# Kernel tuning notes

Measured on AMD Instinct MI355X. Metric: run time of the kernel, lower is better.

Reference implementation:

```python
import jax, jax.numpy as jnp
import numpy as np

B = 64          # batch_size
H = 16384       # n_hidden
BS = 32         # block size of BlockSparseLinear
NB = H // BS    # 512 blocks per dim
NNZ = int(0.1 * NB * NB)  # 26214 nonzero blocks (density 0.1)
N_IN = 1024     # n_inputs
N_OUT = 1024    # n_outputs
STEPS = 8       # n_forward_steps


def setup_inputs() -> dict:
    key = jax.random.key(0)
    k1, k2, k3, k4, k5 = jax.random.split(key, 5)
    # kaiming-ish scale for effective fan-in = H * density
    w_scale = 1.0 / np.sqrt(H * 0.1)
    inp = jax.random.normal(k1, (B, N_IN), dtype=jnp.float32)
    blocks = jax.random.normal(k2, (NNZ, BS, BS), dtype=jnp.float32) * w_scale
    bias = jax.random.normal(k3, (H,), dtype=jnp.float32) * 0.01
    block_rows = jax.random.randint(k4, (NNZ,), 0, NB, dtype=jnp.int32)
    block_cols = jax.random.randint(k5, (NNZ,), 0, NB, dtype=jnp.int32)
    return {"inp": inp, "blocks": blocks, "bias": bias,
            "block_rows": block_rows, "block_cols": block_cols}


def _block_sparse_linear(blocks, block_rows, block_cols, bias, x):
    # x: [B, H] -> y = W_sparse @ x + bias, W stored as NNZ 32x32 blocks
    xb = x.reshape(B, NB, BS)[:, block_cols]               # [B, NNZ, BS]
    contrib = jnp.einsum('nij,bnj->nbi', blocks, xb)       # [NNZ, B, BS]
    yb = jax.ops.segment_sum(contrib, block_rows, num_segments=NB)  # [NB, B, BS]
    return yb.transpose(1, 0, 2).reshape(B, H) + bias


def reference(inp, blocks, bias, block_rows, block_cols):
    # hs = zeros[B, H]; first n_inputs slots get the input (squeeze trailing 1-dim)
    hs = jnp.zeros((B, H), dtype=inp.dtype).at[:, :N_IN].set(inp)
    for step in range(STEPS):
        hs = _block_sparse_linear(blocks, block_rows, block_cols, bias, hs)
        if step != STEPS - 1:
            hs = jax.nn.sigmoid(hs)
    # output_act = sigmoid on last n_outputs entries
    return jax.nn.sigmoid(hs[:, -N_OUT:])
```

## Files before the change

kernel.cpp:

```cpp
#include <hip/hip_runtime.h>
#include <stdint.h>

#define B_     64
#define H_     16384
#define NB_    512
#define NNZ_   26214
#define N_IN_  1024
#define N_OUT_ 1024

typedef __attribute__((ext_vector_type(8))) short    bf16x8;
typedef __attribute__((ext_vector_type(4))) float    f32x4;
typedef __attribute__((ext_vector_type(4))) unsigned int u32x4;

__device__ __forceinline__ unsigned short f2bf(float f) {
    union { unsigned int i; float f; } v; v.f = f;
    unsigned int x = v.i;
    return (unsigned short)((x + 0x7fffu + ((x >> 16) & 1u)) >> 16);
}

__device__ __forceinline__ bf16x8 ldfrag(const unsigned short* p) {
    union { u32x4 u; bf16x8 b; } cv;
    cv.u = *(const u32x4*)p;
    return cv.b;
}


__global__ void zero_cnt(int* __restrict__ cnt) { cnt[threadIdx.x] = 0; }

__global__ void hist(const int* __restrict__ rows, int* __restrict__ cnt) {
    int n = blockIdx.x * 256 + threadIdx.x;
    if (n < NNZ_) atomicAdd(&cnt[rows[n]], 1);
}

__global__ void scan_k(int* __restrict__ cnt, int* __restrict__ ptr) {
    __shared__ int tmp[NB_];
    int t = threadIdx.x;
    tmp[t] = cnt[t];
    __syncthreads();
    for (int off = 1; off < NB_; off <<= 1) {
        int v = (t >= off) ? tmp[t - off] : 0;
        __syncthreads();
        tmp[t] += v;
        __syncthreads();
    }
    if (t == 0) ptr[0] = 0;
    ptr[t + 1] = tmp[t];
    cnt[t] = 0;
}

__global__ void scatter2(const int* __restrict__ rows, const int* __restrict__ cols,
                         const int* __restrict__ ptr, int* __restrict__ cnt,
                         int2* __restrict__ pair2) {
    int n = blockIdx.x * 256 + threadIdx.x;
    if (n < NNZ_) {
        int r = rows[n];
        int pos = ptr[r] + atomicAdd(&cnt[r], 1);
        pair2[pos] = make_int2(n, cols[n]);
    }
}


__global__ __launch_bounds__(256) void conv_w(const float* __restrict__ w,
                                              unsigned short* __restrict__ wb,
                                              const int2* __restrict__ pair2) {
    int pos = blockIdx.x;
    int t   = threadIdx.x;
    int n   = pair2[pos].x;
    f32x4 v = __builtin_nontemporal_load((const f32x4*)(w + (size_t)n * 1024) + t);
    union { unsigned short s[4]; uint2 d; } o;
    o.s[0] = f2bf(v[0]); o.s[1] = f2bf(v[1]); o.s[2] = f2bf(v[2]); o.s[3] = f2bf(v[3]);
    ((uint2*)(wb + (size_t)pos * 1024))[t] = o.d;
}


__global__ __launch_bounds__(256) void init_x(const float* __restrict__ inp,
                                              unsigned short* __restrict__ xb) {
    int idx = blockIdx.x * 256 + threadIdx.x;
    int c = idx >> 11;
    int b = (idx >> 5) & 63;
    int j = idx & 31;
    int h = c * 32 + j;
    xb[idx] = (h < N_IN_) ? f2bf(inp[b * N_IN_ + h]) : (unsigned short)0;
}


#define MFMA8(A, Bv)                                                         \
    do {                                                                     \
        _Pragma("unroll")                                                    \
        for (int mt = 0; mt < 2; ++mt)                                       \
            _Pragma("unroll")                                                \
            for (int nt = 0; nt < 4; ++nt)                                   \
                acc[mt][nt] = __builtin_amdgcn_mfma_f32_16x16x32_bf16(       \
                                  A[mt], Bv[nt], acc[mt][nt], 0, 0, 0);      \
    } while (0)

#define REDUCE_EPILOGUE(LASTF)                                               \
    do {                                                                     \
        if (wv >= 4) {                                                       \
            _Pragma("unroll")                                                \
            for (int mt = 0; mt < 2; ++mt)                                   \
                _Pragma("unroll")                                            \
                for (int nt = 0; nt < 4; ++nt)                               \
                    _Pragma("unroll")                                        \
                    for (int q2 = 0; q2 < 4; ++q2)                           \
                        s_red[wv - 4][nt * 16 + half][mt * 16 + quad * 4 + q2] = \
                            acc[mt][nt][q2];                                 \
        }                                                                    \
        __syncthreads();                                                     \
        if (wv < 4) {                                                        \
            _Pragma("unroll")                                                \
            for (int mt = 0; mt < 2; ++mt)                                   \
                _Pragma("unroll")                                            \
                for (int nt = 0; nt < 4; ++nt)                               \
                    _Pragma("unroll")                                        \
                    for (int q2 = 0; q2 < 4; ++q2)                           \
                        s_red[wv][nt * 16 + half][mt * 16 + quad * 4 + q2] += \
                            acc[mt][nt][q2];                                 \
        }                                                                    \
        __syncthreads();                                                     \
        const int b  = tid >> 3;                                             \
        const int i0 = (tid & 7) * 4;                                        \
        const float4 bv = *(const float4*)&bias[r * 32 + i0];                \
        float v[4] = {bv.x, bv.y, bv.z, bv.w};                               \
        _Pragma("unroll")                                                    \
        for (int w = 0; w < 4; ++w)                                          \
            _Pragma("unroll")                                                \
            for (int k = 0; k < 4; ++k)                                      \
                v[k] += s_red[w][b][i0 + k];                                 \
        if (LASTF) {                                                         \
            float4 o;                                                        \
            o.x = 1.0f / (1.0f + __expf(-v[0]));                             \
            o.y = 1.0f / (1.0f + __expf(-v[1]));                             \
            o.z = 1.0f / (1.0f + __expf(-v[2]));                             \
            o.w = 1.0f / (1.0f + __expf(-v[3]));                             \
            *(float4*)&out[(size_t)b * N_OUT_ +                              \
                           (r - (NB_ - N_OUT_ / 32)) * 32 + i0] = o;         \
        } else {                                                             \
            union { unsigned short s[4]; uint2 u; } o;                       \
            _Pragma("unroll")                                                \
            for (int k = 0; k < 4; ++k)                                      \
                o.s[k] = f2bf(1.0f / (1.0f + __expf(-v[k])));                \
            *(uint2*)&xout[((size_t)r * 64 + b) * 32 + i0] = o.u;            \
        }                                                                    \
    } while (0)


template <bool LAST>
__global__ __launch_bounds__(512, 4) void rowfull_k(
        const unsigned short* __restrict__ x,
        unsigned short* __restrict__ xout,
        float* __restrict__ out,
        const unsigned short* __restrict__ wb,
        const float* __restrict__ bias,
        const int2* __restrict__ pair2,
        const int* __restrict__ ptr,
        int row_base) {
    __shared__ float s_red[4][64][33];

    const int r    = blockIdx.x + row_base;
    const int tid  = threadIdx.x;
    const int wv   = tid >> 6;
    const int lane = tid & 63;
    const int half = lane & 15;
    const int quad = lane >> 4;

    const int beg = ptr[r], cnt = ptr[r + 1] - beg;
    const int c0 = __builtin_amdgcn_readfirstlane(beg + (cnt * wv) / 8);
    const int mv = __builtin_amdgcn_readfirstlane(beg + (cnt * (wv + 1)) / 8 - c0);

    int xoff = 0;
    if (lane < mv) xoff = pair2[c0 + lane].y * 2048;

    const int off16 = half * 32 + quad * 8;
    const unsigned short* wbase = wb + (size_t)c0 * 1024 + off16;

    f32x4 acc[2][4] = {};
    bf16x8 A0[2], B0[4], A1[2], B1[4], A2[2], B2[4];

    #define LDST(A, Bv, t)                                                   \
        do {                                                                 \
            int tt = ((t) < mv - 1) ? (t) : (mv - 1);                        \
            const unsigned short* wp = wbase + (size_t)tt * 1024;            \
            A[0] = ldfrag(wp);                                               \
            A[1] = ldfrag(wp + 512);                                         \
            int xo = __builtin_amdgcn_readlane(xoff, tt);                    \
            const unsigned short* xp = x + xo + off16;                       \
            Bv[0] = ldfrag(xp);                                              \
            Bv[1] = ldfrag(xp + 512);                                        \
            Bv[2] = ldfrag(xp + 1024);                                       \
            Bv[3] = ldfrag(xp + 1536);                                       \
        } while (0)

    if (mv > 0) {
        LDST(A0, B0, 0);
        LDST(A1, B1, 1);
        LDST(A2, B2, 2);
        int j = 0;
        while (j + 3 < mv) {
            MFMA8(A0, B0); LDST(A0, B0, j + 3);
            MFMA8(A1, B1); LDST(A1, B1, j + 4);
            MFMA8(A2, B2); LDST(A2, B2, j + 5);
            j += 3;
        }
        MFMA8(A0, B0);
        if (mv - j > 1) MFMA8(A1, B1);
        if (mv - j > 2) MFMA8(A2, B2);
    }
    #undef LDST

    REDUCE_EPILOGUE(LAST);
}


__global__ __launch_bounds__(512, 4) void rowstep0_k(
        const unsigned short* __restrict__ x,
        unsigned short* __restrict__ xout,
        const unsigned short* __restrict__ wb,
        const float* __restrict__ bias,
        const int2* __restrict__ pair2,
        const int* __restrict__ ptr) {
    __shared__ int2  s_pairs[8][64];
    __shared__ float s_red[4][64][33];
    float* __restrict__ out = nullptr;

    const int r    = blockIdx.x;
    const int tid  = threadIdx.x;
    const int wv   = tid >> 6;
    const int lane = tid & 63;
    const int half = lane & 15;
    const int quad = lane >> 4;

    const int beg = ptr[r], cnt = ptr[r + 1] - beg;
    const int c0 = beg + (cnt * wv) / 8;
    const int m  = beg + (cnt * (wv + 1)) / 8 - c0;

    int2 pc = make_int2(0, 0);
    bool valid = (lane < m);
    if (valid) {
        int c = pair2[c0 + lane].y;
        pc = make_int2(c0 + lane, c);
        valid = (c < N_IN_ / 32);
    }
    unsigned long long mask = __ballot(valid);
    if (valid) {
        int pos = __popcll(mask & ((1ull << lane) - 1ull));
        s_pairs[wv][pos] = pc;
    }
    const int mv = __popcll(mask);

    const int off16 = half * 32 + quad * 8;

    f32x4 acc[2][4] = {};
    bf16x8 A0[2], B0[4], A1[2], B1[4];

    #define LDFRAGS0(A, Bv, p)                                               \
        do {                                                                 \
            const unsigned short* wp = wb + (size_t)(p).x * 1024 + off16;    \
            A[0] = ldfrag(wp);                                               \
            A[1] = ldfrag(wp + 512);                                         \
            const unsigned short* xp = x + (size_t)(p).y * 2048 + off16;     \
            Bv[0] = ldfrag(xp);                                              \
            Bv[1] = ldfrag(xp + 512);                                        \
            Bv[2] = ldfrag(xp + 1024);                                       \
            Bv[3] = ldfrag(xp + 1536);                                       \
        } while (0)

    if (mv > 0) { int2 p = s_pairs[wv][0]; LDFRAGS0(A0, B0, p); }
    int j = 0;
    while (j + 2 <= mv) {
        { int2 p = s_pairs[wv][j + 1]; LDFRAGS0(A1, B1, p); }
        MFMA8(A0, B0);
        if (j + 2 < mv) { int2 p = s_pairs[wv][j + 2]; LDFRAGS0(A0, B0, p); }
        MFMA8(A1, B1);
        j += 2;
    }
    if (j < mv) MFMA8(A0, B0);
    #undef LDFRAGS0

    REDUCE_EPILOGUE(false);
}


extern "C" void kernel_launch(void* const* d_in, const int* in_sizes, int n_in,
                              void* d_out, int out_size, void* d_ws, size_t ws_size,
                              hipStream_t stream) {
    const float* inp    = (const float*)d_in[0];
    const float* blocks = (const float*)d_in[1];
    const float* bias   = (const float*)d_in[2];
    const int*   rows   = (const int*)d_in[3];
    const int*   cols   = (const int*)d_in[4];
    float*       out    = (float*)d_out;

    char* ws = (char*)d_ws;
    unsigned short* wbf = (unsigned short*)ws;
    unsigned short* x0  = (unsigned short*)(ws + 53686272u);
    unsigned short* x1  = (unsigned short*)(ws + 53686272u + 2097152u);
    char*  idxbase      = ws + 53686272u + 2u * 2097152u;
    int*   rowptr = (int*)(idxbase);
    int*   rowcnt = (int*)(idxbase + 4096);
    int2*  pair2  = (int2*)(idxbase + 8192);

    zero_cnt<<<1, NB_, 0, stream>>>(rowcnt);
    hist<<<(NNZ_ + 255) / 256, 256, 0, stream>>>(rows, rowcnt);
    scan_k<<<1, NB_, 0, stream>>>(rowcnt, rowptr);
    scatter2<<<(NNZ_ + 255) / 256, 256, 0, stream>>>(rows, cols, rowptr, rowcnt, pair2);

    conv_w<<<NNZ_, 256, 0, stream>>>(blocks, wbf, pair2);

    init_x<<<(B_ * H_) / 256, 256, 0, stream>>>(inp, x0);

    unsigned short* cur = x0;
    unsigned short* nxt = x1;
    rowstep0_k<<<NB_, 512, 0, stream>>>(cur, nxt, wbf, bias, pair2, rowptr);
    { unsigned short* t = cur; cur = nxt; nxt = t; }
    for (int s = 1; s < 7; ++s) {
        rowfull_k<false><<<NB_, 512, 0, stream>>>(cur, nxt, nullptr, wbf, bias,
                                                  pair2, rowptr, 0);
        unsigned short* t = cur; cur = nxt; nxt = t;
    }
    rowfull_k<true><<<N_OUT_ / 32, 512, 0, stream>>>(cur, nullptr, out, wbf, bias,
                                                     pair2, rowptr,
                                                     NB_ - N_OUT_ / 32);
}
```

Baseline: 311.4 us.

## Fuse all eight recurrent steps into one cooperative kernel with grid barriers

Replaces the per-step kernel launches with a single cooperative persistent kernel (one block per block-row) that loops over the eight steps and uses a hand-written atomic grid barrier between them. The four indexing kernels are merged into one single-block kernel using shared-memory atomics, and weight conversion and input init are merged into one launch. The steady-state pipeline depth also drops from three to two stages. This removes launch gaps and tail effects but relies on all 512 blocks being co-resident, and barrier spin costs may offset the savings.

Measured after the change: 765.2 us. 146% more time.

```diff
diff --git a/kernel.cpp b/kernel.cpp
--- a/kernel.cpp
+++ b/kernel.cpp
@@ -1,4 +1,5 @@
 #include <hip/hip_runtime.h>
+#include <hip/hip_cooperative_groups.h>
 #include <stdint.h>
 
 #define B_     64
@@ -25,62 +26,88 @@
 }
 
 
-__global__ void zero_cnt(int* __restrict__ cnt) { cnt[threadIdx.x] = 0; }
-
-__global__ void hist(const int* __restrict__ rows, int* __restrict__ cnt) {
-    int n = blockIdx.x * 256 + threadIdx.x;
-    if (n < NNZ_) atomicAdd(&cnt[rows[n]], 1);
-}
-
-__global__ void scan_k(int* __restrict__ cnt, int* __restrict__ ptr) {
-    __shared__ int tmp[NB_];
-    int t = threadIdx.x;
-    tmp[t] = cnt[t];
+__global__ __launch_bounds__(1024) void index_k(
+        const int* __restrict__ rows, const int* __restrict__ cols,
+        int* __restrict__ rowptr, int2* __restrict__ pair2,
+        int* __restrict__ bar) {
+    __shared__ int s_cnt[NB_];
+    __shared__ int s_off[NB_];
+    const int t = threadIdx.x;
+
+    if (t < NB_) s_cnt[t] = 0;
+    if (t < 64) bar[t] = 0;
     __syncthreads();
+
+    for (int n = t; n < NNZ_; n += 1024)
+        atomicAdd(&s_cnt[rows[n]], 1);
+    __syncthreads();
+
     for (int off = 1; off < NB_; off <<= 1) {
-        int v = (t >= off) ? tmp[t - off] : 0;
+        int v = 0;
+        if (t < NB_ && t >= off) v = s_cnt[t - off];
         __syncthreads();
-        tmp[t] += v;
+        if (t < NB_) s_cnt[t] += v;
         __syncthreads();
     }
-    if (t == 0) ptr[0] = 0;
-    ptr[t + 1] = tmp[t];
-    cnt[t] = 0;
-}
-
-__global__ void scatter2(const int* __restrict__ rows, const int* __restrict__ cols,
-                         const int* __restrict__ ptr, int* __restrict__ cnt,
-                         int2* __restrict__ pair2) {
-    int n = blockIdx.x * 256 + threadIdx.x;
-    if (n < NNZ_) {
+
+    if (t == 0) rowptr[0] = 0;
+    if (t < NB_) {
+        rowptr[t + 1] = s_cnt[t];
+        s_off[t] = (t == 0) ? 0 : s_cnt[t - 1];
+    }
+    __syncthreads();
+
+    for (int n = t; n < NNZ_; n += 1024) {
         int r = rows[n];
-        int pos = ptr[r] + atomicAdd(&cnt[r], 1);
+        int pos = atomicAdd(&s_off[r], 1);
         pair2[pos] = make_int2(n, cols[n]);
     }
 }
 
 
-__global__ __launch_bounds__(256) void conv_w(const float* __restrict__ w,
-                                              unsigned short* __restrict__ wb,
-                                              const int2* __restrict__ pair2) {
-    int pos = blockIdx.x;
-    int t   = threadIdx.x;
-    int n   = pair2[pos].x;
-    f32x4 v = __builtin_nontemporal_load((const f32x4*)(w + (size_t)n * 1024) + t);
-    union { unsigned short s[4]; uint2 d; } o;
-    o.s[0] = f2bf(v[0]); o.s[1] = f2bf(v[1]); o.s[2] = f2bf(v[2]); o.s[3] = f2bf(v[3]);
-    ((uint2*)(wb + (size_t)pos * 1024))[t] = o.d;
-}
-
-
-__global__ __launch_bounds__(256) void init_x(const float* __restrict__ inp,
-                                              unsigned short* __restrict__ xb) {
-    int idx = blockIdx.x * 256 + threadIdx.x;
-    int c = idx >> 11;
-    int b = (idx >> 5) & 63;
-    int j = idx & 31;
-    int h = c * 32 + j;
-    xb[idx] = (h < N_IN_) ? f2bf(inp[b * N_IN_ + h]) : (unsigned short)0;
+__global__ __launch_bounds__(256) void prep_k(
+        const float* __restrict__ w, unsigned short* __restrict__ wb,
+        const int2* __restrict__ pair2,
+        const float* __restrict__ inp, unsigned short* __restrict__ xb) {
+    const int bb = blockIdx.x;
+    if (bb < NNZ_) {
+        int t = threadIdx.x;
+        int n = pair2[bb].x;
+        f32x4 v = __builtin_nontemporal_load((const f32x4*)(w + (size_t)n * 1024) + t);
+        union { unsigned short s[4]; uint2 d; } o;
+        o.s[0] = f2bf(v[0]); o.s[1] = f2bf(v[1]);
+        o.s[2] = f2bf(v[2]); o.s[3] = f2bf(v[3]);
+        ((uint2*)(wb + (size_t)bb * 1024))[t] = o.d;
+    } else {
+        int idx = (bb - NNZ_) * 256 + threadIdx.x;
+        int c = idx >> 11;
+        int b = (idx >> 5) & 63;
+        int j = idx & 31;
+        int h = c * 32 + j;
+        xb[idx] = (h < N_IN_) ? f2bf(inp[b * N_IN_ + h]) : (unsigned short)0;
+    }
+}
+
+
+__device__ __forceinline__ void gbar(int* bar, int it) {
+    __syncthreads();
+    if (threadIdx.x == 0) {
+        __threadfence();
+        int a = __hip_atomic_fetch_add(&bar[0], 1, __ATOMIC_ACQ_REL,
+                                       __HIP_MEMORY_SCOPE_AGENT);
+        if (a == NB_ - 1) {
+            __hip_atomic_store(&bar[0], 0, __ATOMIC_RELAXED,
+                               __HIP_MEMORY_SCOPE_AGENT);
+            __hip_atomic_store(&bar[32], it + 1, __ATOMIC_RELEASE,
+                               __HIP_MEMORY_SCOPE_AGENT);
+        } else {
+            while (__hip_atomic_load(&bar[32], __ATOMIC_ACQUIRE,
+                                     __HIP_MEMORY_SCOPE_AGENT) <= it)
+                __builtin_amdgcn_s_sleep(2);
+        }
+        __threadfence();
+    }
+    __syncthreads();
 }
 
 
@@ -144,6 +171,119 @@
         }                                                                    \
     } while (0)
 
+#define LDST2(A, Bv, t)                                                      \
+    do {                                                                     \
+        int tt = ((t) < mv - 1) ? (t) : (mv - 1);                            \
+        const unsigned short* wp = wbase + (size_t)tt * 1024;                \
+        A[0] = ldfrag(wp);                                                   \
+        A[1] = ldfrag(wp + 512);                                             \
+        int xo = __builtin_amdgcn_readlane(xoff, tt);                        \
+        const unsigned short* xp = x + xo + off16;                           \
+        Bv[0] = ldfrag(xp);                                                  \
+        Bv[1] = ldfrag(xp + 512);                                            \
+        Bv[2] = ldfrag(xp + 1024);                                           \
+        Bv[3] = ldfrag(xp + 1536);                                           \
+    } while (0)
+
+
+__global__ __launch_bounds__(512, 4) void fused2_k(
+        const unsigned short* __restrict__ xa,
+        unsigned short* __restrict__ xb_,
+        float* __restrict__ out,
+        const unsigned short* __restrict__ wb,
+        const float* __restrict__ bias,
+        const int2* __restrict__ pair2,
+        const int* __restrict__ ptr,
+        int* __restrict__ bar) {
+    __shared__ int2  s_pairs[8][64];
+    __shared__ float s_red[4][64][33];
+
+    const int r    = blockIdx.x;
+    const int tid  = threadIdx.x;
+    const int wv   = tid >> 6;
+    const int lane = tid & 63;
+    const int half = lane & 15;
+    const int quad = lane >> 4;
+
+    const int beg = ptr[r], cnt = ptr[r + 1] - beg;
+    const int c0 = __builtin_amdgcn_readfirstlane(beg + (cnt * wv) / 8);
+    const int mv = __builtin_amdgcn_readfirstlane(beg + (cnt * (wv + 1)) / 8 - c0);
+
+    int pcol = 0;
+    if (lane < mv) pcol = pair2[c0 + lane].y;
+    const int xoff = pcol * 2048;
+
+    const int off16 = half * 32 + quad * 8;
+    const unsigned short* wbase = wb + (size_t)c0 * 1024 + off16;
+
+    {
+        const unsigned short* x = xa;
+        unsigned short* xout = xb_;
+        bool valid = (lane < mv) && (pcol < N_IN_ / 32);
+        unsigned long long mask = __ballot(valid);
+        if (valid) {
+            int pos = __popcll(mask & ((1ull << lane) - 1ull));
+            s_pairs[wv][pos] = make_int2(c0 + lane, pcol);
+        }
+        const int m0 = __popcll(mask);
+
+        f32x4 acc[2][4] = {};
+        bf16x8 A0[2], B0[4], A1[2], B1[4];
+        #define LDP0(A, Bv, p)                                               \
+            do {                                                             \
+                const unsigned short* wp = wb + (size_t)(p).x * 1024 + off16;\
+                A[0] = ldfrag(wp);                                           \
+                A[1] = ldfrag(wp + 512);                                     \
+                const unsigned short* xp = x + (size_t)(p).y * 2048 + off16; \
+                Bv[0] = ldfrag(xp);                                          \
+                Bv[1] = ldfrag(xp + 512);                                    \
+                Bv[2] = ldfrag(xp + 1024);                                   \
+                Bv[3] = ldfrag(xp + 1536);                                   \
+            } while (0)
+        if (m0 > 0) { int2 p = s_pairs[wv][0]; LDP0(A0, B0, p); }
+        int j = 0;
+        while (j + 2 <= m0) {
+            { int2 p = s_pairs[wv][j + 1]; LDP0(A1, B1, p); }
+            MFMA8(A0, B0);
+            if (j + 2 < m0) { int2 p = s_pairs[wv][j + 2]; LDP0(A0, B0, p); }
+            MFMA8(A1, B1);
+            j += 2;
+        }
+        if (j < m0) MFMA8(A0, B0);
+        #undef LDP0
+
+        REDUCE_EPILOGUE(false);
+    }
+    gbar(bar, 0);
+
+    for (int step = 1; step < 8; ++step) {
+        const bool last = (step == 7);
+        if (!last || r >= NB_ - N_OUT_ / 32) {
+            const unsigned short* x = (step & 1) ? xb_ : xa;
+            unsigned short* xout = (step & 1) ? const_cast<unsigned short*>(xa) : xb_;
+
+            f32x4 acc[2][4] = {};
+            bf16x8 A0[2], B0[4], A1[2], B1[4];
+
+            if (mv > 0) {
+                LDST2(A0, B0, 0);
+                LDST2(A1, B1, 1);
+                int j = 0;
+                while (j + 2 < mv) {
+                    MFMA8(A0, B0); LDST2(A0, B0, j + 2);
+                    MFMA8(A1, B1); LDST2(A1, B1, j + 3);
+                    j += 2;
+                }
+                MFMA8(A0, B0);
+                if (mv - j > 1) MFMA8(A1, B1);
+            }
+
+            REDUCE_EPILOGUE(last);
+        }
+        if (step < 7) gbar(bar, step);
+    }
+}
+
 
 template <bool LAST>
 __global__ __launch_bounds__(512, 4) void rowfull_k(
@@ -175,42 +315,23 @@
     const unsigned short* wbase = wb + (size_t)c0 * 1024 + off16;
 
     f32x4 acc[2][4] = {};
-    bf16x8 A0[2], B0[4], A1[2], B1[4], A2[2], B2[4];
-
-    #define LDST(A, Bv, t)                                                   \
-        do {                                                                 \
-            int tt = ((t) < mv - 1) ? (t) : (mv - 1);                        \
-            const unsigned short* wp = wbase + (size_t)tt * 1024;            \
-            A[0] = ldfrag(wp);                                               \
-            A[1] = ldfrag(wp + 512);                                         \
-            int xo = __builtin_amdgcn_readlane(xoff, tt);                    \
-            const unsigned short* xp = x + xo + off16;                       \
-            Bv[0] = ldfrag(xp);                                              \
-            Bv[1] = ldfrag(xp + 512);                                        \
-            Bv[2] = ldfrag(xp + 1024);                                       \
-            Bv[3] = ldfrag(xp + 1536);                                       \
-        } while (0)
+    bf16x8 A0[2], B0[4], A1[2], B1[4];
 
     if (mv > 0) {
-        LDST(A0, B0, 0);
-        LDST(A1, B1, 1);
-        LDST(A2, B2, 2);
+        LDST2(A0, B0, 0);
+        LDST2(A1, B1, 1);
         int j = 0;
-        while (j + 3 < mv) {
-            MFMA8(A0, B0); LDST(A0, B0, j + 3);
-            MFMA8(A1, B1); LDST(A1, B1, j + 4);
-            MFMA8(A2, B2); LDST(A2, B2, j + 5);
-            j += 3;
+        while (j + 2 < mv) {
+            MFMA8(A0, B0); LDST2(A0, B0, j + 2);
+            MFMA8(A1, B1); LDST2(A1, B1, j + 3);
+            j += 2;
         }
         MFMA8(A0, B0);
         if (mv - j > 1) MFMA8(A1, B1);
-        if (mv - j > 2) MFMA8(A2, B2);
-    }
-    #undef LDST
+    }
 
     REDUCE_EPILOGUE(LAST);
 }
-
 
 __global__ __launch_bounds__(512, 4) void rowstep0_k(
         const unsigned short* __restrict__ x,
@@ -253,7 +374,7 @@
     f32x4 acc[2][4] = {};
     bf16x8 A0[2], B0[4], A1[2], B1[4];
 
-    #define LDFRAGS0(A, Bv, p)                                               \
+    #define LDP0(A, Bv, p)                                                   \
         do {                                                                 \
             const unsigned short* wp = wb + (size_t)(p).x * 1024 + off16;    \
             A[0] = ldfrag(wp);                                               \
@@ -264,18 +385,17 @@
             Bv[2] = ldfrag(xp + 1024);                                       \
             Bv[3] = ldfrag(xp + 1536);                                       \
         } while (0)
-
-    if (mv > 0) { int2 p = s_pairs[wv][0]; LDFRAGS0(A0, B0, p); }
+    if (mv > 0) { int2 p = s_pairs[wv][0]; LDP0(A0, B0, p); }
     int j = 0;
     while (j + 2 <= mv) {
-        { int2 p = s_pairs[wv][j + 1]; LDFRAGS0(A1, B1, p); }
+        { int2 p = s_pairs[wv][j + 1]; LDP0(A1, B1, p); }
         MFMA8(A0, B0);
-        if (j + 2 < mv) { int2 p = s_pairs[wv][j + 2]; LDFRAGS0(A0, B0, p); }
+        if (j + 2 < mv) { int2 p = s_pairs[wv][j + 2]; LDP0(A0, B0, p); }
         MFMA8(A1, B1);
         j += 2;
     }
     if (j < mv) MFMA8(A0, B0);
-    #undef LDFRAGS0
+    #undef LDP0
 
     REDUCE_EPILOGUE(false);
 }
@@ -297,28 +417,31 @@
     unsigned short* x1  = (unsigned short*)(ws + 53686272u + 2097152u);
     char*  idxbase      = ws + 53686272u + 2u * 2097152u;
     int*   rowptr = (int*)(idxbase);
-    int*   rowcnt = (int*)(idxbase + 4096);
     int2*  pair2  = (int2*)(idxbase + 8192);
-
-    zero_cnt<<<1, NB_, 0, stream>>>(rowcnt);
-    hist<<<(NNZ_ + 255) / 256, 256, 0, stream>>>(rows, rowcnt);
-    scan_k<<<1, NB_, 0, stream>>>(rowcnt, rowptr);
-    scatter2<<<(NNZ_ + 255) / 256, 256, 0, stream>>>(rows, cols, rowptr, rowcnt, pair2);
-
-    conv_w<<<NNZ_, 256, 0, stream>>>(blocks, wbf, pair2);
-
-    init_x<<<(B_ * H_) / 256, 256, 0, stream>>>(inp, x0);
-
-    unsigned short* cur = x0;
-    unsigned short* nxt = x1;
-    rowstep0_k<<<NB_, 512, 0, stream>>>(cur, nxt, wbf, bias, pair2, rowptr);
-    { unsigned short* t = cur; cur = nxt; nxt = t; }
-    for (int s = 1; s < 7; ++s) {
-        rowfull_k<false><<<NB_, 512, 0, stream>>>(cur, nxt, nullptr, wbf, bias,
-                                                  pair2, rowptr, 0);
-        unsigned short* t = cur; cur = nxt; nxt = t;
-    }
-    rowfull_k<true><<<N_OUT_ / 32, 512, 0, stream>>>(cur, nullptr, out, wbf, bias,
-                                                     pair2, rowptr,
-                                                     NB_ - N_OUT_ / 32);
-}
+    int*   bar    = (int*)(idxbase + 262144);
+
+    index_k<<<1, 1024, 0, stream>>>(rows, cols, rowptr, pair2, bar);
+
+    prep_k<<<NNZ_ + (B_ * H_) / 256, 256, 0, stream>>>(blocks, wbf, pair2, inp, x0);
+
+    void* kargs[] = { (void*)&x0, (void*)&x1, (void*)&out, (void*)&wbf,
+                      (void*)&bias, (void*)&pair2, (void*)&rowptr, (void*)&bar };
+    hipError_t ce = hipLaunchCooperativeKernel(
+        reinterpret_cast<void*>(fused2_k), dim3(NB_), dim3(512), kargs, 0, stream);
+
+    if (ce != hipSuccess) {
+        (void)hipGetLastError();
+        unsigned short* cur = x0;
+        unsigned short* nxt = x1;
+        rowstep0_k<<<NB_, 512, 0, stream>>>(cur, nxt, wbf, bias, pair2, rowptr);
+        { unsigned short* t = cur; cur = nxt; nxt = t; }
+        for (int s = 1; s < 7; ++s) {
+            rowfull_k<false><<<NB_, 512, 0, stream>>>(cur, nxt, nullptr, wbf, bias,
+                                                      pair2, rowptr, 0);
+            unsigned short* t = cur; cur = nxt; nxt = t;
+        }
+        rowfull_k<true><<<N_OUT_ / 32, 512, 0, stream>>>(cur, nullptr, out, wbf,
+                                                         bias, pair2, rowptr,
+                                                         NB_ - N_OUT_ / 32);
+    }
+}
```

## Fuse index build, weight conversion and input init into one prep kernel

Applied to the files above, without the earlier changes.

Replaces six setup launches (zero, histogram, scan, scatter, weight conversion, input init) with a single kernel. Block 0 builds the CSR index in shared memory while the other blocks convert weights and initialise x in parallel. Weights now stay in their original order instead of being permuted by row, so the conversion no longer has to wait for the index build. In exchange, the step kernels gather weight blocks through a per-lane index with readlane rather than reading contiguous per-row blocks, and the main loop drops from triple to double buffering.

Measured after the change: 314.7 us. About the same (+1.0%).

```diff
diff --git a/kernel.cpp b/kernel.cpp
--- a/kernel.cpp
+++ b/kernel.cpp
@@ -7,6 +7,8 @@
 #define NNZ_   26214
 #define N_IN_  1024
 #define N_OUT_ 1024
+#define NCONV_ ((NNZ_ + 3) / 4)
+#define NINIT_ ((B_ * H_) / 1024)
 
 typedef __attribute__((ext_vector_type(8))) short    bf16x8;
 typedef __attribute__((ext_vector_type(4))) float    f32x4;
@@ -25,62 +27,59 @@
 }
 
 
-__global__ void zero_cnt(int* __restrict__ cnt) { cnt[threadIdx.x] = 0; }
-
-__global__ void hist(const int* __restrict__ rows, int* __restrict__ cnt) {
-    int n = blockIdx.x * 256 + threadIdx.x;
-    if (n < NNZ_) atomicAdd(&cnt[rows[n]], 1);
-}
-
-__global__ void scan_k(int* __restrict__ cnt, int* __restrict__ ptr) {
-    __shared__ int tmp[NB_];
-    int t = threadIdx.x;
-    tmp[t] = cnt[t];
-    __syncthreads();
-    for (int off = 1; off < NB_; off <<= 1) {
-        int v = (t >= off) ? tmp[t - off] : 0;
+__global__ __launch_bounds__(1024) void prepidx_k(
+        const int* __restrict__ rows, const int* __restrict__ cols,
+        int* __restrict__ rowptr, int2* __restrict__ pair2,
+        const float* __restrict__ w, unsigned short* __restrict__ wb,
+        const float* __restrict__ inp, unsigned short* __restrict__ xb) {
+    const int bb = blockIdx.x;
+    const int t  = threadIdx.x;
+
+    if (bb == 0) {
+        __shared__ int s_cnt[NB_];
+        __shared__ int s_off[NB_];
+        if (t < NB_) s_cnt[t] = 0;
         __syncthreads();
-        tmp[t] += v;
+        for (int n = t; n < NNZ_; n += 1024)
+            atomicAdd(&s_cnt[rows[n]], 1);
         __syncthreads();
-    }
-    if (t == 0) ptr[0] = 0;
-    ptr[t + 1] = tmp[t];
-    cnt[t] = 0;
-}
-
-__global__ void scatter2(const int* __restrict__ rows, const int* __restrict__ cols,
-                         const int* __restrict__ ptr, int* __restrict__ cnt,
-                         int2* __restrict__ pair2) {
-    int n = blockIdx.x * 256 + threadIdx.x;
-    if (n < NNZ_) {
-        int r = rows[n];
-        int pos = ptr[r] + atomicAdd(&cnt[r], 1);
-        pair2[pos] = make_int2(n, cols[n]);
-    }
-}
-
-
-__global__ __launch_bounds__(256) void conv_w(const float* __restrict__ w,
-                                              unsigned short* __restrict__ wb,
-                                              const int2* __restrict__ pair2) {
-    int pos = blockIdx.x;
-    int t   = threadIdx.x;
-    int n   = pair2[pos].x;
-    f32x4 v = __builtin_nontemporal_load((const f32x4*)(w + (size_t)n * 1024) + t);
-    union { unsigned short s[4]; uint2 d; } o;
-    o.s[0] = f2bf(v[0]); o.s[1] = f2bf(v[1]); o.s[2] = f2bf(v[2]); o.s[3] = f2bf(v[3]);
-    ((uint2*)(wb + (size_t)pos * 1024))[t] = o.d;
-}
-
-
-__global__ __launch_bounds__(256) void init_x(const float* __restrict__ inp,
-                                              unsigned short* __restrict__ xb) {
-    int idx = blockIdx.x * 256 + threadIdx.x;
-    int c = idx >> 11;
-    int b = (idx >> 5) & 63;
-    int j = idx & 31;
-    int h = c * 32 + j;
-    xb[idx] = (h < N_IN_) ? f2bf(inp[b * N_IN_ + h]) : (unsigned short)0;
+        for (int off = 1; off < NB_; off <<= 1) {
+            int v = 0;
+            if (t < NB_ && t >= off) v = s_cnt[t - off];
+            __syncthreads();
+            if (t < NB_) s_cnt[t] += v;
+            __syncthreads();
+        }
+        if (t == 0) rowptr[0] = 0;
+        if (t < NB_) {
+            rowptr[t + 1] = s_cnt[t];
+            s_off[t] = (t == 0) ? 0 : s_cnt[t - 1];
+        }
+        __syncthreads();
+        for (int n = t; n < NNZ_; n += 1024) {
+            int r = rows[n];
+            int pos = atomicAdd(&s_off[r], 1);
+            pair2[pos] = make_int2(n, cols[n]);
+        }
+    } else if (bb <= NCONV_) {
+        int n = (bb - 1) * 4 + (t >> 8);
+        if (n < NNZ_) {
+            int q = t & 255;
+            f32x4 v = __builtin_nontemporal_load(
+                          (const f32x4*)(w + (size_t)n * 1024) + q);
+            union { unsigned short s[4]; uint2 d; } o;
+            o.s[0] = f2bf(v[0]); o.s[1] = f2bf(v[1]);
+            o.s[2] = f2bf(v[2]); o.s[3] = f2bf(v[3]);
+            ((uint2*)(wb + (size_t)n * 1024))[q] = o.d;
+        }
+    } else {
+        int idx = (bb - NCONV_ - 1) * 1024 + t;
+        int c = idx >> 11;
+        int b = (idx >> 5) & 63;
+        int j = idx & 31;
+        int h = c * 32 + j;
+        xb[idx] = (h < N_IN_) ? f2bf(inp[b * N_IN_ + h]) : (unsigned short)0;
+    }
 }
 
 
@@ -144,6 +143,21 @@
         }                                                                    \
     } while (0)
 
+#define LDST2(A, Bv, t)                                                      \
+    do {                                                                     \
+        int tt = ((t) < mv - 1) ? (t) : (mv - 1);                            \
+        int nn = __builtin_amdgcn_readlane(nidx, tt);                        \
+        const unsigned short* wp = wb + (size_t)nn * 1024 + off16;           \
+        A[0] = ldfrag(wp);                                                   \
+        A[1] = ldfrag(wp + 512);                                             \
+        int xo = __builtin_amdgcn_readlane(xoff, tt);                        \
+        const unsigned short* xp = x + xo + off16;                           \
+        Bv[0] = ldfrag(xp);                                                  \
+        Bv[1] = ldfrag(xp + 512);                                            \
+        Bv[2] = ldfrag(xp + 1024);                                           \
+        Bv[3] = ldfrag(xp + 1536);                                           \
+    } while (0)
+
 
 template <bool LAST>
 __global__ __launch_bounds__(512, 4) void rowfull_k(
@@ -168,45 +182,30 @@
     const int c0 = __builtin_amdgcn_readfirstlane(beg + (cnt * wv) / 8);
     const int mv = __builtin_amdgcn_readfirstlane(beg + (cnt * (wv + 1)) / 8 - c0);
 
-    int xoff = 0;
-    if (lane < mv) xoff = pair2[c0 + lane].y * 2048;
+    int nidx = 0, xoff = 0;
+    if (lane < mv) {
+        int2 p = pair2[c0 + lane];
+        nidx = p.x;
+        xoff = p.y * 2048;
+    }
 
     const int off16 = half * 32 + quad * 8;
-    const unsigned short* wbase = wb + (size_t)c0 * 1024 + off16;
 
     f32x4 acc[2][4] = {};
-    bf16x8 A0[2], B0[4], A1[2], B1[4], A2[2], B2[4];
-
-    #define LDST(A, Bv, t)                                                   \
-        do {                                                                 \
-            int tt = ((t) < mv - 1) ? (t) : (mv - 1);                        \
-            const unsigned short* wp = wbase + (size_t)tt * 1024;            \
-            A[0] = ldfrag(wp);                                               \
-            A[1] = ldfrag(wp + 512);                                         \
-            int xo = __builtin_amdgcn_readlane(xoff, tt);                    \
-            const unsigned short* xp = x + xo + off16;                       \
-            Bv[0] = ldfrag(xp);                                              \
-            Bv[1] = ldfrag(xp + 512);                                        \
-            Bv[2] = ldfrag(xp + 1024);                                       \
-            Bv[3] = ldfrag(xp + 1536);                                       \
-        } while (0)
+    bf16x8 A0[2], B0[4], A1[2], B1[4];
 
     if (mv > 0) {
-        LDST(A0, B0, 0);
-        LDST(A1, B1, 1);
-        LDST(A2, B2, 2);
+        LDST2(A0, B0, 0);
+        LDST2(A1, B1, 1);
         int j = 0;
-        while (j + 3 < mv) {
-            MFMA8(A0, B0); LDST(A0, B0, j + 3);
-            MFMA8(A1, B1); LDST(A1, B1, j + 4);
-            MFMA8(A2, B2); LDST(A2, B2, j + 5);
-            j += 3;
+        while (j + 2 < mv) {
+            MFMA8(A0, B0); LDST2(A0, B0, j + 2);
+            MFMA8(A1, B1); LDST2(A1, B1, j + 3);
+            j += 2;
         }
         MFMA8(A0, B0);
         if (mv - j > 1) MFMA8(A1, B1);
-        if (mv - j > 2) MFMA8(A2, B2);
-    }
-    #undef LDST
+    }
 
     REDUCE_EPILOGUE(LAST);
 }
@@ -237,9 +236,9 @@
     int2 pc = make_int2(0, 0);
     bool valid = (lane < m);
     if (valid) {
-        int c = pair2[c0 + lane].y;
-        pc = make_int2(c0 + lane, c);
-        valid = (c < N_IN_ / 32);
+        int2 p = pair2[c0 + lane];
+        pc = p;
+        valid = (p.y < N_IN_ / 32);
     }
     unsigned long long mask = __ballot(valid);
     if (valid) {
@@ -253,7 +252,7 @@
     f32x4 acc[2][4] = {};
     bf16x8 A0[2], B0[4], A1[2], B1[4];
 
-    #define LDFRAGS0(A, Bv, p)                                               \
+    #define LDP0(A, Bv, p)                                                   \
         do {                                                                 \
             const unsigned short* wp = wb + (size_t)(p).x * 1024 + off16;    \
             A[0] = ldfrag(wp);                                               \
@@ -264,18 +263,17 @@
             Bv[2] = ldfrag(xp + 1024);                                       \
             Bv[3] = ldfrag(xp + 1536);                                       \
         } while (0)
-
-    if (mv > 0) { int2 p = s_pairs[wv][0]; LDFRAGS0(A0, B0, p); }
+    if (mv > 0) { int2 p = s_pairs[wv][0]; LDP0(A0, B0, p); }
     int j = 0;
     while (j + 2 <= mv) {
-        { int2 p = s_pairs[wv][j + 1]; LDFRAGS0(A1, B1, p); }
+        { int2 p = s_pairs[wv][j + 1]; LDP0(A1, B1, p); }
         MFMA8(A0, B0);
-        if (j + 2 < mv) { int2 p = s_pairs[wv][j + 2]; LDFRAGS0(A0, B0, p); }
+        if (j + 2 < mv) { int2 p = s_pairs[wv][j + 2]; LDP0(A0, B0, p); }
         MFMA8(A1, B1);
         j += 2;
     }
     if (j < mv) MFMA8(A0, B0);
-    #undef LDFRAGS0
+    #undef LDP0
 
     REDUCE_EPILOGUE(false);
 }
@@ -297,17 +295,10 @@
     unsigned short* x1  = (unsigned short*)(ws + 53686272u + 2097152u);
     char*  idxbase      = ws + 53686272u + 2u * 2097152u;
     int*   rowptr = (int*)(idxbase);
-    int*   rowcnt = (int*)(idxbase + 4096);
     int2*  pair2  = (int2*)(idxbase + 8192);
 
-    zero_cnt<<<1, NB_, 0, stream>>>(rowcnt);
-    hist<<<(NNZ_ + 255) / 256, 256, 0, stream>>>(rows, rowcnt);
-    scan_k<<<1, NB_, 0, stream>>>(rowcnt, rowptr);
-    scatter2<<<(NNZ_ + 255) / 256, 256, 0, stream>>>(rows, cols, rowptr, rowcnt, pair2);
-
-    conv_w<<<NNZ_, 256, 0, stream>>>(blocks, wbf, pair2);
-
-    init_x<<<(B_ * H_) / 256, 256, 0, stream>>>(inp, x0);
+    prepidx_k<<<1 + NCONV_ + NINIT_, 1024, 0, stream>>>(
+        rows, cols, rowptr, pair2, blocks, wbf, inp, x0);
 
     unsigned short* cur = x0;
     unsigned short* nxt = x1;
```
